# Kernel tuning notes

Hardware: AMD Instinct MI355X
Metric: run time of the kernel (lower is better)

The kernel has to match this reference:

```python
import jax, jax.numpy as jnp
import numpy as np

HIDDEN = 256
NUM_LEVELS = 4
BATCH = 256
NUM_SLOTS = 64
NUM_FEATURES = 4096


def setup_inputs() -> dict:
    key = jax.random.key(0)
    ks = jax.random.split(key, 6)
    s = 1.0 / np.sqrt(HIDDEN)
    return {
        "attention_weights": jax.random.uniform(ks[0], (BATCH, NUM_SLOTS, NUM_FEATURES), dtype=jnp.float32),
        "current_centers": jax.random.normal(ks[1], (NUM_FEATURES, HIDDEN), dtype=jnp.float32),
        "w_ih": jax.random.uniform(ks[2], (3 * HIDDEN, HIDDEN), jnp.float32, -s, s),
        "w_hh": jax.random.uniform(ks[3], (3 * HIDDEN, HIDDEN), jnp.float32, -s, s),
        "b_ih": jax.random.uniform(ks[4], (3 * HIDDEN,), jnp.float32, -s, s),
        "b_hh": jax.random.uniform(ks[5], (3 * HIDDEN,), jnp.float32, -s, s),
        "num_levels": NUM_LEVELS,
    }


def reference(attention_weights, current_centers, w_ih, w_hh, b_ih, b_hh, num_levels):
    B, S, F = attention_weights.shape
    H = current_centers.shape[1]
    O = S // num_levels  # num_objects

    # aggregated features: bmm with shared center matrix -> [B, S, H]
    x = jnp.einsum("bsf,fh->bsh", attention_weights, current_centers)

    # per-slot hidden state: slot i*L+j uses current_centers[i] -> [S, H]
    h = jnp.repeat(current_centers[:O], num_levels, axis=0)

    # fused GRUCell gates over all (batch, slot) pairs (torch gate order: r, z, n)
    gi = x @ w_ih.T + b_ih            # [B, S, 3H]
    gh = h @ w_hh.T + b_hh            # [S, 3H], broadcasts over batch
    gi_r, gi_z, gi_n = jnp.split(gi, 3, axis=-1)
    gh_r, gh_z, gh_n = jnp.split(gh, 3, axis=-1)

    r = jax.nn.sigmoid(gi_r + gh_r)
    z = jax.nn.sigmoid(gi_z + gh_z)
    n = jnp.tanh(gi_n + r * gh_n)
    h_new = (1.0 - z) * n + z * h     # [B, S, H]

    # average the num_levels updates per object, then stack objects first
    out = h_new.reshape(B, O, num_levels, H).mean(axis=2)  # [B, O, H]
    return jnp.transpose(out, (1, 0, 2))                   # [O, B, H]
```

## Files before the change

kernel.cpp:

```cpp
#include <hip/hip_runtime.h>
#include <stdint.h>


typedef _Float16 half8 __attribute__((ext_vector_type(8)));
typedef float f32x4 __attribute__((ext_vector_type(4)));

#define WS_CT   0u
#define WS_WP   2097152u
#define WS_GH   2490368u
#define WS_CSP  2686976u
#define WS_CS   2752512u
#define WS_CSW  2753536u
#define WS_X    2756608u

static __device__ __forceinline__ _Float16 f2h(float x) {
  return (_Float16)x;
}
static __device__ __forceinline__ void gload16(const void* g, void* lds) {
  __builtin_amdgcn_global_load_lds(
      (const __attribute__((address_space(1))) unsigned int*)g,
      (__attribute__((address_space(3))) unsigned int*)lds, 16, 0, 0);
}
static __device__ __forceinline__ float sigmf(float x) {
  float e = __expf(-fabsf(x));
  float p = 1.f / (1.f + e);
  return x >= 0.f ? p : 1.f - p;
}
static __device__ __forceinline__ float tanhf2(float x) {
  float e = __expf(-2.f * fabsf(x));
  float t = 1.f - 2.f * e / (1.f + e);
  return x >= 0.f ? t : -t;
}

__global__ void __launch_bounds__(256) k_transC(const float* __restrict__ C,
                                                _Float16* __restrict__ Ct) {
  __shared__ float sT[64][65];
  const int f0 = blockIdx.x * 64, h0 = blockIdx.y * 64;
  const int t = threadIdx.x;
#pragma unroll
  for (int i = 0; i < 4; ++i) {
    int fl = t + 256 * i;
    int r = fl >> 4, c4 = fl & 15;
    float4 v = *(const float4*)(C + (size_t)(f0 + r) * 256 + h0 + c4 * 4);
    sT[r][c4 * 4 + 0] = v.x; sT[r][c4 * 4 + 1] = v.y;
    sT[r][c4 * 4 + 2] = v.z; sT[r][c4 * 4 + 3] = v.w;
  }
  __syncthreads();
#pragma unroll
  for (int i = 0; i < 2; ++i) {
    int q = t + 256 * i;
    int hr = q >> 3, j = q & 7;
    int h = h0 + hr;
    union { half8 v; _Float16 u[8]; } pk;
#pragma unroll
    for (int u = 0; u < 8; ++u) pk.u[u] = f2h(sT[j * 8 + u][hr]);
    size_t off = (size_t)h * 8192 + (size_t)f0 * 2 + (size_t)((j ^ (h & 7)) << 4);
    *(half8*)((char*)Ct + off) = pk.v;
  }
}

__global__ void __launch_bounds__(256) k_csum(const float* __restrict__ C,
                                              float* __restrict__ part) {
  const int b = blockIdx.x, t = threadIdx.x;
  float s = 0.f;
  for (int k = 0; k < 64; ++k) s += C[(size_t)(b * 64 + k) * 256 + t];
  part[b * 256 + t] = s;
}
__global__ void __launch_bounds__(256) k_csum2(const float* __restrict__ part,
                                               float* __restrict__ csum) {
  const int t = threadIdx.x;
  float s = 0.f;
#pragma unroll
  for (int b = 0; b < 64; ++b) s += part[b * 256 + t];
  csum[t] = 0.5f * s;
}
__global__ void __launch_bounds__(256) k_csumW(const float* __restrict__ w_ih,
                                               const float* __restrict__ cs,
                                               float* __restrict__ csW) {
  const int wv = threadIdx.x >> 6, l = threadIdx.x & 63;
  const int n = blockIdx.x * 4 + wv;
  float4 w = *(const float4*)(w_ih + (size_t)n * 256 + l * 4);
  float4 c = *(const float4*)(cs + l * 4);
  float s = w.x * c.x + w.y * c.y + w.z * c.z + w.w * c.w;
#pragma unroll
  for (int off = 32; off; off >>= 1) s += __shfl_down(s, off, 64);
  if (l == 0) csW[n] = s;
}

__global__ void __launch_bounds__(256) k_prepWp(const float* __restrict__ w_ih,
                                                _Float16* __restrict__ Wp) {
  int q = blockIdx.x * 256 + threadIdx.x;
  int row = q >> 5, c = q & 31;
  int seg = c >> 3, j = c & 7;
  int srow = (row % 3) * 256 + row / 3;
  const float* src = w_ih + (size_t)srow * 256 + c * 8;
  union { half8 v; _Float16 u[8]; } pk;
#pragma unroll
  for (int u = 0; u < 8; ++u) pk.u[u] = f2h(src[u]);
  size_t off = (size_t)row * 512 + seg * 128 + ((j ^ (row & 7)) << 4);
  *(half8*)((char*)Wp + off) = pk.v;
}

__global__ void __launch_bounds__(256) k_gh(const float* __restrict__ centers,
                                            const float* __restrict__ w_hh,
                                            const float* __restrict__ b_hh,
                                            float* __restrict__ GH) {
  __shared__ __align__(16) float sH[256];
  const int s = blockIdx.x, t = threadIdx.x;
  sH[t] = centers[(size_t)(s >> 2) * 256 + t];
  __syncthreads();
#pragma unroll
  for (int e = 0; e < 3; ++e) {
    int n = e * 256 + t;
    float accv = b_hh[n];
    const float4* w = (const float4*)(w_hh + (size_t)n * 256);
#pragma unroll 8
    for (int k = 0; k < 64; ++k) {
      float4 v = w[k];
      float4 hh = *(const float4*)&sH[k * 4];
      accv += v.x * hh.x + v.y * hh.y + v.z * hh.z + v.w * hh.w;
    }
    GH[(size_t)s * 768 + n] = accv;
  }
}

__global__ void __launch_bounds__(256, 1) k_stage1(const float* __restrict__ A,
                                                   const _Float16* __restrict__ Ct,
                                                   _Float16* __restrict__ X) {
  __shared__ __align__(16) _Float16 sA0[64 * 64];
  __shared__ __align__(16) _Float16 sA1[64 * 64];
  __shared__ __align__(16) _Float16 sB0[256 * 64];
  __shared__ __align__(16) _Float16 sB1[256 * 64];
  const int t = threadIdx.x;
  const int wid = t >> 6, l = t & 63;
  const int lr = l & 15, lk = l >> 4;
  const int m0 = blockIdx.x * 64;

  f32x4 acc[4][4];
#pragma unroll
  for (int i = 0; i < 4; ++i)
#pragma unroll
    for (int j = 0; j < 4; ++j) acc[i][j] = (f32x4){0.f, 0.f, 0.f, 0.f};

  const int ar = t >> 2, ac4 = t & 3;
  const float* aptr = A + (size_t)(m0 + ar) * 4096 + ac4 * 16;
  const int saw0 = ar * 128 + (((2 * ac4 + 0) ^ (ar & 7)) << 4);
  const int saw1 = ar * 128 + (((2 * ac4 + 1) ^ (ar & 7)) << 4);

  const int brow = t >> 3, bch = t & 7;

#pragma unroll
  for (int i = 0; i < 8; ++i)
    gload16(Ct + (size_t)(brow + 32 * i) * 4096 + bch * 8,
            (char*)sB0 + (wid * 64 + 256 * i) * 16);
  f32x4 aEv[4], aOd[4];
#pragma unroll
  for (int j = 0; j < 4; ++j)
    aEv[j] = __builtin_nontemporal_load((const f32x4*)(aptr + j * 4));
#pragma unroll
  for (int j = 0; j < 4; ++j)
    aOd[j] = __builtin_nontemporal_load((const f32x4*)(aptr + 64 + j * 4));

  auto ITER = [&](int kk, f32x4* areg, _Float16* sAc, _Float16* sBc,
                  _Float16* sBn) {
    asm volatile("s_waitcnt vmcnt(0)" ::: "memory");
    {
      union { half8 v; _Float16 u[8]; } w0, w1;
      w0.u[0] = f2h(areg[0].x - 0.5f); w0.u[1] = f2h(areg[0].y - 0.5f);
      w0.u[2] = f2h(areg[0].z - 0.5f); w0.u[3] = f2h(areg[0].w - 0.5f);
      w0.u[4] = f2h(areg[1].x - 0.5f); w0.u[5] = f2h(areg[1].y - 0.5f);
      w0.u[6] = f2h(areg[1].z - 0.5f); w0.u[7] = f2h(areg[1].w - 0.5f);
      w1.u[0] = f2h(areg[2].x - 0.5f); w1.u[1] = f2h(areg[2].y - 0.5f);
      w1.u[2] = f2h(areg[2].z - 0.5f); w1.u[3] = f2h(areg[2].w - 0.5f);
      w1.u[4] = f2h(areg[3].x - 0.5f); w1.u[5] = f2h(areg[3].y - 0.5f);
      w1.u[6] = f2h(areg[3].z - 0.5f); w1.u[7] = f2h(areg[3].w - 0.5f);
      *(half8*)((char*)sAc + saw0) = w0.v;
      *(half8*)((char*)sAc + saw1) = w1.v;
    }
    if (kk <= 61) {
      const float* ap = aptr + (kk + 2) * 64;
#pragma unroll
      for (int j = 0; j < 4; ++j)
        areg[j] = __builtin_nontemporal_load((const f32x4*)(ap + j * 4));
    }
    if (kk <= 62) {
#pragma unroll
      for (int i = 0; i < 8; ++i)
        gload16(Ct + (size_t)(brow + 32 * i) * 4096 + (size_t)(kk + 1) * 64 + bch * 8,
                (char*)sBn + (wid * 64 + 256 * i) * 16);
    }
    asm volatile("s_waitcnt lgkmcnt(0)" ::: "memory");
    __builtin_amdgcn_s_barrier();
    asm volatile("" ::: "memory");
#pragma unroll
    for (int kc = 0; kc < 2; ++kc) {
      const int q = kc * 4 + lk;
      half8 af[4], bf[4];
#pragma unroll
      for (int mi = 0; mi < 4; ++mi) {
        int rl = mi * 16 + lr;
        af[mi] = *(const half8*)((const char*)sAc + rl * 128 + ((q ^ (rl & 7)) << 4));
      }
#pragma unroll
      for (int ni = 0; ni < 4; ++ni) {
        int rb = wid * 64 + ni * 16 + lr;
        bf[ni] = *(const half8*)((const char*)sBc + rb * 128 + ((q ^ (rb & 7)) << 4));
      }
#pragma unroll
      for (int mi = 0; mi < 4; ++mi)
#pragma unroll
        for (int ni = 0; ni < 4; ++ni)
          acc[mi][ni] = __builtin_amdgcn_mfma_f32_16x16x32_f16(af[mi], bf[ni], acc[mi][ni], 0, 0, 0);
    }
    asm volatile("" ::: "memory");
    __builtin_amdgcn_s_barrier();
    asm volatile("" ::: "memory");
  };

  for (int kx = 0; kx < 64; kx += 2) {
    ITER(kx + 0, aEv, sA0, sB0, sB1);
    ITER(kx + 1, aOd, sA1, sB1, sB0);
  }

#pragma unroll
  for (int mi = 0; mi < 4; ++mi)
#pragma unroll
    for (int ni = 0; ni < 4; ++ni)
#pragma unroll
      for (int p = 0; p < 4; ++p) {
        int m = m0 + mi * 16 + lk * 4 + p;
        int col = wid * 64 + ni * 16 + lr;
        size_t off = (size_t)m * 512 + ((col >> 6) << 7) +
                     ((((col >> 3) & 7) ^ (m & 7)) << 4) + ((col & 7) << 1);
        *(_Float16*)((char*)X + off) = f2h(acc[mi][ni][p]);
      }
}

__global__ void __launch_bounds__(256) k_stage2(const _Float16* __restrict__ X,
                                                const _Float16* __restrict__ Wp,
                                                const float* __restrict__ GH,
                                                const float* __restrict__ centers,
                                                const float* __restrict__ b_ih,
                                                const float* __restrict__ csW,
                                                float* __restrict__ out) {
  __shared__ __align__(16) char smem[81920];
  _Float16* sX = (_Float16*)smem;
  char*     sW = smem + 32768;
  float*    sC = (float*)(smem + 32768);
  const int t = threadIdx.x;
  const int wid = t >> 6, l = t & 63;
  const int lr = l & 15, lk = l >> 4;
  const int wm = wid >> 1, wn = wid & 1;
  const int b = blockIdx.x;

#pragma unroll
  for (int i = 0; i < 8; ++i) {
    int flat = t + 256 * i;
    gload16((const char*)X + ((size_t)b * 64 + (flat >> 5)) * 512 +
                (size_t)(flat & 31) * 16,
            (char*)sX + (wid * 64 + 256 * i) * 16);
  }
  __syncthreads();

  for (int nt = 0; nt < 8; ++nt) {
    const int n0 = nt * 96;
    f32x4 acc[2][3];
#pragma unroll
    for (int i = 0; i < 2; ++i)
#pragma unroll
      for (int j = 0; j < 3; ++j) acc[i][j] = (f32x4){0.f, 0.f, 0.f, 0.f};

#pragma unroll
    for (int i = 0; i < 12; ++i) {
      int flat = t + 256 * i;
      gload16((const char*)Wp + (size_t)(n0 + (flat >> 5)) * 512 +
                  (size_t)(flat & 31) * 16,
              sW + (wid * 64 + 256 * i) * 16);
    }
    __syncthreads();
#pragma unroll
    for (int kc = 0; kc < 8; ++kc) {
      const int q = kc * 4 + lk;
      const int seg = (q >> 3) << 7, jj = q & 7;
      half8 af[2];
#pragma unroll
      for (int mi = 0; mi < 2; ++mi) {
        int rl = wm * 32 + mi * 16 + lr;
        af[mi] = *(const half8*)((const char*)sX + rl * 512 + seg + ((jj ^ (rl & 7)) << 4));
      }
#pragma unroll
      for (int ni = 0; ni < 3; ++ni) {
        int rw = wn * 48 + ni * 16 + lr;
        half8 bf = *(const half8*)(sW + rw * 512 + seg + ((jj ^ (rw & 7)) << 4));
#pragma unroll
        for (int mi = 0; mi < 2; ++mi)
          acc[mi][ni] = __builtin_amdgcn_mfma_f32_16x16x32_f16(af[mi], bf, acc[mi][ni], 0, 0, 0);
      }
    }
    __syncthreads();
#pragma unroll
    for (int mi = 0; mi < 2; ++mi)
#pragma unroll
      for (int ni = 0; ni < 3; ++ni)
#pragma unroll
        for (int p = 0; p < 4; ++p) {
          int row = wm * 32 + mi * 16 + lk * 4 + p;
          int col = wn * 48 + ni * 16 + lr;
          sC[row * 100 + col] = acc[mi][ni][p];
        }
    __syncthreads();
#pragma unroll
    for (int ii = 0; ii < 2; ++ii) {
      int item = t + 256 * ii;
      int hl = item & 31, o = item >> 5;
      int h = nt * 32 + hl;
      float hprev = centers[o * 256 + h];
      float bir = b_ih[h] + csW[h];
      float biz = b_ih[256 + h] + csW[256 + h];
      float bin = b_ih[512 + h] + csW[512 + h];
      float sum = 0.f;
#pragma unroll
      for (int j = 0; j < 4; ++j) {
        int s = 4 * o + j;
        float gir = sC[s * 100 + 3 * hl + 0] + bir;
        float giz = sC[s * 100 + 3 * hl + 1] + biz;
        float gin = sC[s * 100 + 3 * hl + 2] + bin;
        float rg = sigmf(gir + GH[s * 768 + h]);
        float zg = sigmf(giz + GH[s * 768 + 256 + h]);
        float ng = tanhf2(gin + rg * GH[s * 768 + 512 + h]);
        sum += (1.f - zg) * ng + zg * hprev;
      }
      out[(size_t)o * 65536 + (size_t)b * 256 + h] = 0.25f * sum;
    }
    __syncthreads();
  }
}

extern "C" void kernel_launch(void* const* d_in, const int* in_sizes, int n_in,
                              void* d_out, int out_size, void* d_ws, size_t ws_size,
                              hipStream_t stream) {
  (void)in_sizes; (void)n_in; (void)out_size; (void)ws_size;
  const float* attn    = (const float*)d_in[0];
  const float* centers = (const float*)d_in[1];
  const float* w_ih    = (const float*)d_in[2];
  const float* w_hh    = (const float*)d_in[3];
  const float* b_ih    = (const float*)d_in[4];
  const float* b_hh    = (const float*)d_in[5];

  char* ws = (char*)d_ws;
  _Float16* Ct  = (_Float16*)(ws + WS_CT);
  _Float16* Wpp = (_Float16*)(ws + WS_WP);
  float*    GHp = (float*)(ws + WS_GH);
  float*    csp = (float*)(ws + WS_CSP);
  float*    cs  = (float*)(ws + WS_CS);
  float*    csW = (float*)(ws + WS_CSW);
  _Float16* X   = (_Float16*)(ws + WS_X);
  float* out = (float*)d_out;

  hipLaunchKernelGGL(k_transC, dim3(64, 4), dim3(256), 0, stream, centers, Ct);
  hipLaunchKernelGGL(k_csum, dim3(64), dim3(256), 0, stream, centers, csp);
  hipLaunchKernelGGL(k_csum2, dim3(1), dim3(256), 0, stream, csp, cs);
  hipLaunchKernelGGL(k_csumW, dim3(192), dim3(256), 0, stream, w_ih, cs, csW);
  hipLaunchKernelGGL(k_prepWp, dim3(96), dim3(256), 0, stream, w_ih, Wpp);
  hipLaunchKernelGGL(k_gh, dim3(64), dim3(256), 0, stream, centers, w_hh, b_hh, GHp);
  hipLaunchKernelGGL(k_stage1, dim3(256), dim3(256), 0, stream, attn, Ct, X);
  hipLaunchKernelGGL(k_stage2, dim3(256), dim3(256), 0, stream, X, Wpp, GHp, centers, b_ih, csW, out);
}
```

Measured before the change: 195.6 us.

## Halve stage1 M-tile, double grid, and restructure to single-barrier pipeline

The stage1 GEMM tile shrinks from 64 to 32 rows, so the grid doubles to 512 blocks and the launch bound asks for 2 blocks per CU. This is meant to fill the 256 CUs better and raise occupancy. The loop body now uses one barrier per iteration instead of two. It issues the next B-tile and A loads after the barrier, writes the converted A for the next step into the alternate LDS buffer, and uses a partial vmcnt wait so loads overlap with the MFMAs. In exchange, the Ct tile is read twice as often across blocks, and the new wait-count and double-buffer ordering is delicate to get right.

```diff
diff --git a/kernel.cpp b/kernel.cpp
--- a/kernel.cpp
+++ b/kernel.cpp
@@ -124,80 +124,84 @@
   }
 }
 
-__global__ void __launch_bounds__(256, 1) k_stage1(const float* __restrict__ A,
+__global__ void __launch_bounds__(256, 2) k_stage1(const float* __restrict__ A,
                                                    const _Float16* __restrict__ Ct,
                                                    _Float16* __restrict__ X) {
-  __shared__ __align__(16) _Float16 sA0[64 * 64];
-  __shared__ __align__(16) _Float16 sA1[64 * 64];
+  __shared__ __align__(16) _Float16 sA0[32 * 64];
+  __shared__ __align__(16) _Float16 sA1[32 * 64];
   __shared__ __align__(16) _Float16 sB0[256 * 64];
   __shared__ __align__(16) _Float16 sB1[256 * 64];
   const int t = threadIdx.x;
   const int wid = t >> 6, l = t & 63;
   const int lr = l & 15, lk = l >> 4;
-  const int m0 = blockIdx.x * 64;
-
-  f32x4 acc[4][4];
-#pragma unroll
-  for (int i = 0; i < 4; ++i)
+  const int m0 = blockIdx.x * 32;
+
+  f32x4 acc[2][4];
+#pragma unroll
+  for (int i = 0; i < 2; ++i)
 #pragma unroll
     for (int j = 0; j < 4; ++j) acc[i][j] = (f32x4){0.f, 0.f, 0.f, 0.f};
 
-  const int ar = t >> 2, ac4 = t & 3;
-  const float* aptr = A + (size_t)(m0 + ar) * 4096 + ac4 * 16;
-  const int saw0 = ar * 128 + (((2 * ac4 + 0) ^ (ar & 7)) << 4);
-  const int saw1 = ar * 128 + (((2 * ac4 + 1) ^ (ar & 7)) << 4);
-
-  const int brow = t >> 3, bch = t & 7;
+  const int ar = t >> 3, aj = t & 7;
+  const float* aptr = A + (size_t)(m0 + ar) * 4096 + aj * 8;
+  const int saw = ar * 128 + ((aj ^ (ar & 7)) << 4);
+
+  const int br = t >> 3, bj = t & 7;
+
+  f32x4 aEv[2], aOd[2];
 
 #pragma unroll
   for (int i = 0; i < 8; ++i)
-    gload16(Ct + (size_t)(brow + 32 * i) * 4096 + bch * 8,
+    gload16(Ct + (size_t)(br + 32 * i) * 4096 + bj * 8,
             (char*)sB0 + (wid * 64 + 256 * i) * 16);
-  f32x4 aEv[4], aOd[4];
-#pragma unroll
-  for (int j = 0; j < 4; ++j)
-    aEv[j] = __builtin_nontemporal_load((const f32x4*)(aptr + j * 4));
-#pragma unroll
-  for (int j = 0; j < 4; ++j)
-    aOd[j] = __builtin_nontemporal_load((const f32x4*)(aptr + 64 + j * 4));
-
-  auto ITER = [&](int kk, f32x4* areg, _Float16* sAc, _Float16* sBc,
-                  _Float16* sBn) {
-    asm volatile("s_waitcnt vmcnt(0)" ::: "memory");
-    {
-      union { half8 v; _Float16 u[8]; } w0, w1;
-      w0.u[0] = f2h(areg[0].x - 0.5f); w0.u[1] = f2h(areg[0].y - 0.5f);
-      w0.u[2] = f2h(areg[0].z - 0.5f); w0.u[3] = f2h(areg[0].w - 0.5f);
-      w0.u[4] = f2h(areg[1].x - 0.5f); w0.u[5] = f2h(areg[1].y - 0.5f);
-      w0.u[6] = f2h(areg[1].z - 0.5f); w0.u[7] = f2h(areg[1].w - 0.5f);
-      w1.u[0] = f2h(areg[2].x - 0.5f); w1.u[1] = f2h(areg[2].y - 0.5f);
-      w1.u[2] = f2h(areg[2].z - 0.5f); w1.u[3] = f2h(areg[2].w - 0.5f);
-      w1.u[4] = f2h(areg[3].x - 0.5f); w1.u[5] = f2h(areg[3].y - 0.5f);
-      w1.u[6] = f2h(areg[3].z - 0.5f); w1.u[7] = f2h(areg[3].w - 0.5f);
-      *(half8*)((char*)sAc + saw0) = w0.v;
-      *(half8*)((char*)sAc + saw1) = w1.v;
+  aEv[0] = __builtin_nontemporal_load((const f32x4*)(aptr));
+  aEv[1] = __builtin_nontemporal_load((const f32x4*)(aptr + 4));
+  aOd[0] = __builtin_nontemporal_load((const f32x4*)(aptr + 64));
+  aOd[1] = __builtin_nontemporal_load((const f32x4*)(aptr + 64 + 4));
+  {
+    union { half8 v; _Float16 u[8]; } pk;
+    pk.u[0] = f2h(aEv[0].x - 0.5f); pk.u[1] = f2h(aEv[0].y - 0.5f);
+    pk.u[2] = f2h(aEv[0].z - 0.5f); pk.u[3] = f2h(aEv[0].w - 0.5f);
+    pk.u[4] = f2h(aEv[1].x - 0.5f); pk.u[5] = f2h(aEv[1].y - 0.5f);
+    pk.u[6] = f2h(aEv[1].z - 0.5f); pk.u[7] = f2h(aEv[1].w - 0.5f);
+    *(half8*)((char*)sA0 + saw) = pk.v;
+  }
+
+  auto body = [&](int kk, const _Float16* sAc, const _Float16* sBc,
+                  _Float16* sAn, _Float16* sBn, f32x4* aWr, f32x4* aLd) {
+    if (kk == 63) {
+      asm volatile("s_waitcnt vmcnt(0)" ::: "memory");
+    } else {
+      asm volatile("s_waitcnt vmcnt(2)" ::: "memory");
+    }
+    asm volatile("s_waitcnt lgkmcnt(0)" ::: "memory");
+    __builtin_amdgcn_s_barrier();
+    __builtin_amdgcn_sched_barrier(0);
+    if (kk <= 62) {
+#pragma unroll
+      for (int i = 0; i < 8; ++i)
+        gload16(Ct + (size_t)(br + 32 * i) * 4096 + (size_t)(kk + 1) * 64 + bj * 8,
+                (char*)sBn + (wid * 64 + 256 * i) * 16);
     }
     if (kk <= 61) {
       const float* ap = aptr + (kk + 2) * 64;
-#pragma unroll
-      for (int j = 0; j < 4; ++j)
-        areg[j] = __builtin_nontemporal_load((const f32x4*)(ap + j * 4));
+      aLd[0] = __builtin_nontemporal_load((const f32x4*)(ap));
+      aLd[1] = __builtin_nontemporal_load((const f32x4*)(ap + 4));
     }
     if (kk <= 62) {
-#pragma unroll
-      for (int i = 0; i < 8; ++i)
-        gload16(Ct + (size_t)(brow + 32 * i) * 4096 + (size_t)(kk + 1) * 64 + bch * 8,
-                (char*)sBn + (wid * 64 + 256 * i) * 16);
-    }
-    asm volatile("s_waitcnt lgkmcnt(0)" ::: "memory");
-    __builtin_amdgcn_s_barrier();
-    asm volatile("" ::: "memory");
+      union { half8 v; _Float16 u[8]; } pk;
+      pk.u[0] = f2h(aWr[0].x - 0.5f); pk.u[1] = f2h(aWr[0].y - 0.5f);
+      pk.u[2] = f2h(aWr[0].z - 0.5f); pk.u[3] = f2h(aWr[0].w - 0.5f);
+      pk.u[4] = f2h(aWr[1].x - 0.5f); pk.u[5] = f2h(aWr[1].y - 0.5f);
+      pk.u[6] = f2h(aWr[1].z - 0.5f); pk.u[7] = f2h(aWr[1].w - 0.5f);
+      *(half8*)((char*)sAn + saw) = pk.v;
+    }
 #pragma unroll
     for (int kc = 0; kc < 2; ++kc) {
       const int q = kc * 4 + lk;
-      half8 af[4], bf[4];
-#pragma unroll
-      for (int mi = 0; mi < 4; ++mi) {
+      half8 af[2], bf[4];
+#pragma unroll
+      for (int mi = 0; mi < 2; ++mi) {
         int rl = mi * 16 + lr;
         af[mi] = *(const half8*)((const char*)sAc + rl * 128 + ((q ^ (rl & 7)) << 4));
       }
@@ -207,23 +211,20 @@
         bf[ni] = *(const half8*)((const char*)sBc + rb * 128 + ((q ^ (rb & 7)) << 4));
       }
 #pragma unroll
-      for (int mi = 0; mi < 4; ++mi)
+      for (int mi = 0; mi < 2; ++mi)
 #pragma unroll
         for (int ni = 0; ni < 4; ++ni)
           acc[mi][ni] = __builtin_amdgcn_mfma_f32_16x16x32_f16(af[mi], bf[ni], acc[mi][ni], 0, 0, 0);
     }
-    asm volatile("" ::: "memory");
-    __builtin_amdgcn_s_barrier();
-    asm volatile("" ::: "memory");
   };
 
   for (int kx = 0; kx < 64; kx += 2) {
-    ITER(kx + 0, aEv, sA0, sB0, sB1);
-    ITER(kx + 1, aOd, sA1, sB1, sB0);
-  }
-
-#pragma unroll
-  for (int mi = 0; mi < 4; ++mi)
+    body(kx + 0, sA0, sB0, sA1, sB1, aOd, aEv);
+    body(kx + 1, sA1, sB1, sA0, sB0, aEv, aOd);
+  }
+
+#pragma unroll
+  for (int mi = 0; mi < 2; ++mi)
 #pragma unroll
     for (int ni = 0; ni < 4; ++ni)
 #pragma unroll
@@ -363,6 +364,6 @@
   hipLaunchKernelGGL(k_csumW, dim3(192), dim3(256), 0, stream, w_ih, cs, csW);
   hipLaunchKernelGGL(k_prepWp, dim3(96), dim3(256), 0, stream, w_ih, Wpp);
   hipLaunchKernelGGL(k_gh, dim3(64), dim3(256), 0, stream, centers, w_hh, b_hh, GHp);
-  hipLaunchKernelGGL(k_stage1, dim3(256), dim3(256), 0, stream, attn, Ct, X);
+  hipLaunchKernelGGL(k_stage1, dim3(512), dim3(256), 0, stream, attn, Ct, X);
   hipLaunchKernelGGL(k_stage2, dim3(256), dim3(256), 0, stream, X, Wpp, GHp, centers, b_ih, csW, out);
 }
```

Result: faster. 167.4 us (-14.4%).

## Retile stage1 GEMM to 128x128 tiles with 512 threads and single-barrier pipeline

Applied to the files above, without the earlier changes.

Stage1 moves from 64x256 output tiles with 4 waves to 128x128 tiles with 8 waves. Each block now covers half the N dimension, and blocks are remapped so the two N halves of an M tile are scheduled close together. The K loop drops from two barriers to one: the next A tile is converted and written into the other buffer while MFMAs run, with a partial vmcnt wait. The aim is better overlap and more waves per CU, at the cost of each A row being read twice from HBM (once per N half), which the block ordering tries to serve from L2.

```diff
diff --git a/kernel.cpp b/kernel.cpp
--- a/kernel.cpp
+++ b/kernel.cpp
@@ -124,112 +124,136 @@
   }
 }
 
-__global__ void __launch_bounds__(256, 1) k_stage1(const float* __restrict__ A,
+__global__ void __launch_bounds__(512, 1) k_stage1(const float* __restrict__ A,
                                                    const _Float16* __restrict__ Ct,
                                                    _Float16* __restrict__ X) {
-  __shared__ __align__(16) _Float16 sA0[64 * 64];
-  __shared__ __align__(16) _Float16 sA1[64 * 64];
-  __shared__ __align__(16) _Float16 sB0[256 * 64];
-  __shared__ __align__(16) _Float16 sB1[256 * 64];
+  __shared__ __align__(16) _Float16 sA0[128 * 64];
+  __shared__ __align__(16) _Float16 sA1[128 * 64];
+  __shared__ __align__(16) _Float16 sB0[128 * 64];
+  __shared__ __align__(16) _Float16 sB1[128 * 64];
   const int t = threadIdx.x;
   const int wid = t >> 6, l = t & 63;
   const int lr = l & 15, lk = l >> 4;
-  const int m0 = blockIdx.x * 64;
-
-  f32x4 acc[4][4];
+  const int wm = wid >> 2, wn = wid & 3;
+  const int wgid = blockIdx.x;
+  const int nh = (wgid >> 3) & 1;
+  const int mt = (wgid & 7) | ((wgid >> 4) << 3);
+  const int m0 = mt * 128;
+  const int n0 = nh * 128;
+
+  f32x4 acc[4][2];
 #pragma unroll
   for (int i = 0; i < 4; ++i)
 #pragma unroll
-    for (int j = 0; j < 4; ++j) acc[i][j] = (f32x4){0.f, 0.f, 0.f, 0.f};
-
-  const int ar = t >> 2, ac4 = t & 3;
-  const float* aptr = A + (size_t)(m0 + ar) * 4096 + ac4 * 16;
-  const int saw0 = ar * 128 + (((2 * ac4 + 0) ^ (ar & 7)) << 4);
-  const int saw1 = ar * 128 + (((2 * ac4 + 1) ^ (ar & 7)) << 4);
-
-  const int brow = t >> 3, bch = t & 7;
-
-#pragma unroll
-  for (int i = 0; i < 8; ++i)
-    gload16(Ct + (size_t)(brow + 32 * i) * 4096 + bch * 8,
-            (char*)sB0 + (wid * 64 + 256 * i) * 16);
+    for (int j = 0; j < 2; ++j) acc[i][j] = (f32x4){0.f, 0.f, 0.f, 0.f};
+
+  const int ar = t >> 2, aq = t & 3;
+  const float* aptr = A + (size_t)(m0 + ar) * 4096 + aq * 16;
+  const int sw0 = ar * 128 + (((2 * aq + 0) ^ (ar & 7)) << 4);
+  const int sw1 = ar * 128 + (((2 * aq + 1) ^ (ar & 7)) << 4);
+
+  const int br = t >> 3, bj = t & 7;
+
   f32x4 aEv[4], aOd[4];
+
+#pragma unroll
+  for (int i = 0; i < 2; ++i) {
+    int row = br + 64 * i;
+    gload16(Ct + (size_t)(n0 + row) * 4096 + bj * 8,
+            (char*)sB0 + (t + 512 * i) * 16);
+  }
 #pragma unroll
   for (int j = 0; j < 4; ++j)
     aEv[j] = __builtin_nontemporal_load((const f32x4*)(aptr + j * 4));
 #pragma unroll
   for (int j = 0; j < 4; ++j)
     aOd[j] = __builtin_nontemporal_load((const f32x4*)(aptr + 64 + j * 4));
-
-  auto ITER = [&](int kk, f32x4* areg, _Float16* sAc, _Float16* sBc,
-                  _Float16* sBn) {
-    asm volatile("s_waitcnt vmcnt(0)" ::: "memory");
-    {
-      union { half8 v; _Float16 u[8]; } w0, w1;
-      w0.u[0] = f2h(areg[0].x - 0.5f); w0.u[1] = f2h(areg[0].y - 0.5f);
-      w0.u[2] = f2h(areg[0].z - 0.5f); w0.u[3] = f2h(areg[0].w - 0.5f);
-      w0.u[4] = f2h(areg[1].x - 0.5f); w0.u[5] = f2h(areg[1].y - 0.5f);
-      w0.u[6] = f2h(areg[1].z - 0.5f); w0.u[7] = f2h(areg[1].w - 0.5f);
-      w1.u[0] = f2h(areg[2].x - 0.5f); w1.u[1] = f2h(areg[2].y - 0.5f);
-      w1.u[2] = f2h(areg[2].z - 0.5f); w1.u[3] = f2h(areg[2].w - 0.5f);
-      w1.u[4] = f2h(areg[3].x - 0.5f); w1.u[5] = f2h(areg[3].y - 0.5f);
-      w1.u[6] = f2h(areg[3].z - 0.5f); w1.u[7] = f2h(areg[3].w - 0.5f);
-      *(half8*)((char*)sAc + saw0) = w0.v;
-      *(half8*)((char*)sAc + saw1) = w1.v;
+  {
+    union { half8 v; _Float16 u[8]; } w0, w1;
+    w0.u[0] = f2h(aEv[0].x - 0.5f); w0.u[1] = f2h(aEv[0].y - 0.5f);
+    w0.u[2] = f2h(aEv[0].z - 0.5f); w0.u[3] = f2h(aEv[0].w - 0.5f);
+    w0.u[4] = f2h(aEv[1].x - 0.5f); w0.u[5] = f2h(aEv[1].y - 0.5f);
+    w0.u[6] = f2h(aEv[1].z - 0.5f); w0.u[7] = f2h(aEv[1].w - 0.5f);
+    w1.u[0] = f2h(aEv[2].x - 0.5f); w1.u[1] = f2h(aEv[2].y - 0.5f);
+    w1.u[2] = f2h(aEv[2].z - 0.5f); w1.u[3] = f2h(aEv[2].w - 0.5f);
+    w1.u[4] = f2h(aEv[3].x - 0.5f); w1.u[5] = f2h(aEv[3].y - 0.5f);
+    w1.u[6] = f2h(aEv[3].z - 0.5f); w1.u[7] = f2h(aEv[3].w - 0.5f);
+    *(half8*)((char*)sA0 + sw0) = w0.v;
+    *(half8*)((char*)sA0 + sw1) = w1.v;
+  }
+
+  auto body = [&](int kk, const _Float16* sAc, const _Float16* sBc,
+                  _Float16* sAn, _Float16* sBn, f32x4* aWr, f32x4* aLd) {
+    if (kk == 63) {
+      asm volatile("s_waitcnt vmcnt(0)" ::: "memory");
+    } else {
+      asm volatile("s_waitcnt vmcnt(4)" ::: "memory");
+    }
+    asm volatile("s_waitcnt lgkmcnt(0)" ::: "memory");
+    __builtin_amdgcn_s_barrier();
+    __builtin_amdgcn_sched_barrier(0);
+    if (kk <= 62) {
+#pragma unroll
+      for (int i = 0; i < 2; ++i) {
+        int row = br + 64 * i;
+        gload16(Ct + (size_t)(n0 + row) * 4096 + (size_t)(kk + 1) * 64 + bj * 8,
+                (char*)sBn + (t + 512 * i) * 16);
+      }
     }
     if (kk <= 61) {
       const float* ap = aptr + (kk + 2) * 64;
 #pragma unroll
       for (int j = 0; j < 4; ++j)
-        areg[j] = __builtin_nontemporal_load((const f32x4*)(ap + j * 4));
+        aLd[j] = __builtin_nontemporal_load((const f32x4*)(ap + j * 4));
     }
     if (kk <= 62) {
-#pragma unroll
-      for (int i = 0; i < 8; ++i)
-        gload16(Ct + (size_t)(brow + 32 * i) * 4096 + (size_t)(kk + 1) * 64 + bch * 8,
-                (char*)sBn + (wid * 64 + 256 * i) * 16);
-    }
-    asm volatile("s_waitcnt lgkmcnt(0)" ::: "memory");
-    __builtin_amdgcn_s_barrier();
-    asm volatile("" ::: "memory");
+      union { half8 v; _Float16 u[8]; } w0, w1;
+      w0.u[0] = f2h(aWr[0].x - 0.5f); w0.u[1] = f2h(aWr[0].y - 0.5f);
+      w0.u[2] = f2h(aWr[0].z - 0.5f); w0.u[3] = f2h(aWr[0].w - 0.5f);
+      w0.u[4] = f2h(aWr[1].x - 0.5f); w0.u[5] = f2h(aWr[1].y - 0.5f);
+      w0.u[6] = f2h(aWr[1].z - 0.5f); w0.u[7] = f2h(aWr[1].w - 0.5f);
+      w1.u[0] = f2h(aWr[2].x - 0.5f); w1.u[1] = f2h(aWr[2].y - 0.5f);
+      w1.u[2] = f2h(aWr[2].z - 0.5f); w1.u[3] = f2h(aWr[2].w - 0.5f);
+      w1.u[4] = f2h(aWr[3].x - 0.5f); w1.u[5] = f2h(aWr[3].y - 0.5f);
+      w1.u[6] = f2h(aWr[3].z - 0.5f); w1.u[7] = f2h(aWr[3].w - 0.5f);
+      *(half8*)((char*)sAn + sw0) = w0.v;
+      *(half8*)((char*)sAn + sw1) = w1.v;
+    }
 #pragma unroll
     for (int kc = 0; kc < 2; ++kc) {
       const int q = kc * 4 + lk;
-      half8 af[4], bf[4];
+      half8 af[4], bf[2];
 #pragma unroll
       for (int mi = 0; mi < 4; ++mi) {
-        int rl = mi * 16 + lr;
+        int rl = wm * 64 + mi * 16 + lr;
         af[mi] = *(const half8*)((const char*)sAc + rl * 128 + ((q ^ (rl & 7)) << 4));
       }
 #pragma unroll
-      for (int ni = 0; ni < 4; ++ni) {
-        int rb = wid * 64 + ni * 16 + lr;
+      for (int ni = 0; ni < 2; ++ni) {
+        int rb = wn * 32 + ni * 16 + lr;
         bf[ni] = *(const half8*)((const char*)sBc + rb * 128 + ((q ^ (rb & 7)) << 4));
       }
 #pragma unroll
       for (int mi = 0; mi < 4; ++mi)
 #pragma unroll
-        for (int ni = 0; ni < 4; ++ni)
+        for (int ni = 0; ni < 2; ++ni)
           acc[mi][ni] = __builtin_amdgcn_mfma_f32_16x16x32_f16(af[mi], bf[ni], acc[mi][ni], 0, 0, 0);
     }
-    asm volatile("" ::: "memory");
-    __builtin_amdgcn_s_barrier();
-    asm volatile("" ::: "memory");
   };
 
   for (int kx = 0; kx < 64; kx += 2) {
-    ITER(kx + 0, aEv, sA0, sB0, sB1);
-    ITER(kx + 1, aOd, sA1, sB1, sB0);
+    body(kx + 0, sA0, sB0, sA1, sB1, aOd, aEv);
+    body(kx + 1, sA1, sB1, sA0, sB0, aEv, aOd);
   }
 
 #pragma unroll
   for (int mi = 0; mi < 4; ++mi)
 #pragma unroll
-    for (int ni = 0; ni < 4; ++ni)
+    for (int ni = 0; ni < 2; ++ni)
 #pragma unroll
       for (int p = 0; p < 4; ++p) {
-        int m = m0 + mi * 16 + lk * 4 + p;
-        int col = wid * 64 + ni * 16 + lr;
+        int m = m0 + wm * 64 + mi * 16 + lk * 4 + p;
+        int col = n0 + wn * 32 + ni * 16 + lr;
         size_t off = (size_t)m * 512 + ((col >> 6) << 7) +
                      ((((col >> 3) & 7) ^ (m & 7)) << 4) + ((col & 7) << 1);
         *(_Float16*)((char*)X + off) = f2h(acc[mi][ni][p]);
@@ -363,6 +387,6 @@
   hipLaunchKernelGGL(k_csumW, dim3(192), dim3(256), 0, stream, w_ih, cs, csW);
   hipLaunchKernelGGL(k_prepWp, dim3(96), dim3(256), 0, stream, w_ih, Wpp);
   hipLaunchKernelGGL(k_gh, dim3(64), dim3(256), 0, stream, centers, w_hh, b_hh, GHp);
-  hipLaunchKernelGGL(k_stage1, dim3(256), dim3(256), 0, stream, attn, Ct, X);
+  hipLaunchKernelGGL(k_stage1, dim3(256), dim3(512), 0, stream, attn, Ct, X);
   hipLaunchKernelGGL(k_stage2, dim3(256), dim3(256), 0, stream, X, Wpp, GHp, centers, b_ih, csW, out);
 }
```

After: 228.3 us. 1.17x slower.
